# Performance work log

Measured on AMD Instinct MI355X. Metric: run time of the kernel, lower is better.

Reference implementation:

```python
import jax, jax.numpy as jnp
import numpy as np

HIDDEN = 2048
NUM_HEADS = 32
NUM_KV_HEADS = 8
HEAD_DIM = 64
HEADS_PER_KV = NUM_HEADS // NUM_KV_HEADS


def setup_inputs() -> dict:
    key = jax.random.key(0)
    ks = jax.random.split(key, 5)
    B, S = 2, 2048
    sd = 1.0 / np.sqrt(HIDDEN)
    x = jax.random.normal(ks[0], (B, S, HIDDEN), dtype=jnp.float32)
    wq = jax.random.normal(ks[1], (HIDDEN, NUM_HEADS * HEAD_DIM), dtype=jnp.float32) * sd
    wk = jax.random.normal(ks[2], (HIDDEN, NUM_KV_HEADS * HEAD_DIM), dtype=jnp.float32) * sd
    wv = jax.random.normal(ks[3], (HIDDEN, NUM_KV_HEADS * HEAD_DIM), dtype=jnp.float32) * sd
    wo = jax.random.normal(ks[4], (NUM_HEADS * HEAD_DIM, HIDDEN), dtype=jnp.float32) * sd
    return {"x": x, "wq": wq, "wk": wk, "wv": wv, "wo": wo}


def reference(x, wq, wk, wv, wo):
    B, S, _ = x.shape
    scale = 1.0 / np.sqrt(HEAD_DIM)
    # projections; self-attention (is_cross=False) so kv source = x
    q = (x @ wq).reshape(B, S, NUM_HEADS, HEAD_DIM)          # [B,S,H,D]
    k = (x @ wk).reshape(B, S, NUM_KV_HEADS, HEAD_DIM)        # [B,S,Hkv,D]
    v = (x @ wv).reshape(B, S, NUM_KV_HEADS, HEAD_DIM)
    # GQA: group query heads per kv head instead of repeating K/V
    q = q.reshape(B, S, NUM_KV_HEADS, HEADS_PER_KV, HEAD_DIM)
    # scores: [B, Hkv, G, Sq, Skv]
    scores = jnp.einsum('bqhgd,bkhd->bhgqk', q, k) * scale
    probs = jax.nn.softmax(scores, axis=-1)
    out = jnp.einsum('bhgqk,bkhd->bqhgd', probs, v)
    out = out.reshape(B, S, NUM_HEADS * HEAD_DIM)
    return out @ wo
```

## Files before the change

kernel.cpp:

```cpp
#include <hip/hip_runtime.h>
#include <hip/hip_bf16.h>


#define S_LEN 2048

typedef __hip_bfloat16 bf16;
using bf16x8 = __attribute__((ext_vector_type(8))) __bf16;
using f32x4  = __attribute__((ext_vector_type(4))) float;

__device__ inline unsigned short bf16_bits(float f) {
    union { __hip_bfloat16 h; unsigned short u; } cv;
    cv.h = __float2bfloat16(f);
    return cv.u;
}

__device__ inline float bits_to_f(unsigned short u) {
    union { __hip_bfloat16 h; unsigned short u; } cv;
    cv.u = u;
    return __bfloat162float(cv.h);
}

__device__ inline unsigned int cvt_pk_bf16(float lo, float hi) {
    unsigned int r;
    asm volatile("v_cvt_pk_bf16_f32 %0, %1, %2" : "=v"(r) : "v"(lo), "v"(hi));
    return r;
}

__device__ inline bf16x8 load_cvt8(const float* __restrict__ p) {
    f32x4 a = *(const f32x4*)p;
    f32x4 b = *(const f32x4*)(p + 4);
    union { bf16x8 v; unsigned short u[8]; } r;
    r.u[0] = bf16_bits(a[0]); r.u[1] = bf16_bits(a[1]);
    r.u[2] = bf16_bits(a[2]); r.u[3] = bf16_bits(a[3]);
    r.u[4] = bf16_bits(b[0]); r.u[5] = bf16_bits(b[1]);
    r.u[6] = bf16_bits(b[2]); r.u[7] = bf16_bits(b[3]);
    return r.v;
}

__device__ inline void gload_lds16(const bf16* g, bf16* l) {
    __builtin_amdgcn_global_load_lds((const __attribute__((address_space(1))) void*)g,
                                     (__attribute__((address_space(3))) void*)l,
                                     16, 0, 0);
}

__global__ __launch_bounds__(256) void prep_k(const float* __restrict__ x,
                                              const float* __restrict__ wq,
                                              const float* __restrict__ wk,
                                              const float* __restrict__ wv,
                                              bf16* __restrict__ xb,
                                              bf16* __restrict__ wqT,
                                              bf16* __restrict__ wkT,
                                              bf16* __restrict__ wvT) {
    __shared__ float tile[32][33];
    int bid = blockIdx.x;
    if (bid < 4096) {
        int i = bid * 256 + threadIdx.x;
        *(bf16x8*)(xb + (size_t)i * 8) = load_cvt8(x + (size_t)i * 8);
        return;
    }
    const float* in; bf16* out; int R, C, local;
    if (bid < 8192)      { local = bid - 4096; in = wq; out = wqT; R = 2048; C = 2048; }
    else if (bid < 9216) { local = bid - 8192; in = wk; out = wkT; R = 2048; C = 512;  }
    else                 { local = bid - 9216; in = wv; out = wvT; R = 2048; C = 512;  }
    int gx = C >> 5;
    int c0 = (local % gx) * 32, r0 = (local / gx) * 32;
    int tx = threadIdx.x & 31, ty = threadIdx.x >> 5;
#pragma unroll
    for (int p = 0; p < 4; ++p)
        tile[ty + p * 8][tx] = in[(size_t)(r0 + ty + p * 8) * C + c0 + tx];
    __syncthreads();
#pragma unroll
    for (int p = 0; p < 4; ++p)
        out[(size_t)(c0 + ty + p * 8) * R + r0 + tx] = __float2bfloat16(tile[tx][ty + p * 8]);
}

__global__ __launch_bounds__(256) void transpose_k(const float* __restrict__ in,
                                                   bf16* __restrict__ out,
                                                   int R, int C) {
    __shared__ float tile[32][33];
    int tx = threadIdx.x & 31, ty = threadIdx.x >> 5;
    int r0 = blockIdx.y * 32, c0 = blockIdx.x * 32;
#pragma unroll
    for (int p = 0; p < 4; ++p)
        tile[ty + p * 8][tx] = in[(size_t)(r0 + ty + p * 8) * C + c0 + tx];
    __syncthreads();
#pragma unroll
    for (int p = 0; p < 4; ++p)
        out[(size_t)(c0 + ty + p * 8) * R + r0 + tx] = __float2bfloat16(tile[tx][ty + p * 8]);
}

__global__ __launch_bounds__(256) void gemm_k(const bf16* __restrict__ A,
                                              const bf16* __restrict__ Bt,
                                              void* __restrict__ Cv,
                                              void* __restrict__ Cv2,
                                              void* __restrict__ Cv3,
                                              int M, int N, int K, int mode) {
    __shared__ bf16 As[128 * 32];
    __shared__ bf16 Bs[128 * 32];
    int tid  = threadIdx.x;
    int lane = tid & 63, wave = tid >> 6;
    int quad = lane >> 4, r = lane & 15;
    int wm = (wave >> 1) * 64, wn = (wave & 1) * 64;

    int nwg  = gridDim.x * gridDim.y;
    int flat = blockIdx.y * gridDim.x + blockIdx.x;
    int cpx  = nwg >> 3;
    int swz  = (flat & 7) * cpx + (flat >> 3);
    int m0 = (swz / gridDim.x) * 128, n0 = (swz % gridDim.x) * 128;

    f32x4 acc[4][4];
#pragma unroll
    for (int i = 0; i < 4; ++i)
#pragma unroll
        for (int j = 0; j < 4; ++j) acc[i][j] = (f32x4)0.0f;

    int rg = lane >> 2;
    int ck = (lane & 3) << 3;

    for (int k0 = 0; k0 < K; k0 += 32) {
#pragma unroll
        for (int g = 0; g < 2; ++g) {
            int grp = wave * 2 + g;
            int row = grp * 16 + rg;
            gload_lds16(A  + (size_t)(m0 + row) * K + k0 + ck, &As[grp * 512]);
            gload_lds16(Bt + (size_t)(n0 + row) * K + k0 + ck, &Bs[grp * 512]);
        }
        __syncthreads();
        bf16x8 af[4], bfr[4];
#pragma unroll
        for (int mt = 0; mt < 4; ++mt) af[mt]  = *(const bf16x8*)&As[(wm + mt * 16 + r) * 32 + quad * 8];
#pragma unroll
        for (int nt = 0; nt < 4; ++nt) bfr[nt] = *(const bf16x8*)&Bs[(wn + nt * 16 + r) * 32 + quad * 8];
#pragma unroll
        for (int mt = 0; mt < 4; ++mt)
#pragma unroll
            for (int nt = 0; nt < 4; ++nt)
                acc[mt][nt] = __builtin_amdgcn_mfma_f32_16x16x32_bf16(af[mt], bfr[nt], acc[mt][nt], 0, 0, 0);
        __syncthreads();
    }

    if (mode == 2) {
        float* C = (float*)Cv;
#pragma unroll
        for (int mt = 0; mt < 4; ++mt)
#pragma unroll
            for (int nt = 0; nt < 4; ++nt) {
                int row = m0 + wm + mt * 16 + quad * 4;
                int col = n0 + wn + nt * 16 + r;
#pragma unroll
                for (int i = 0; i < 4; ++i)
                    C[(size_t)(row + i) * N + col] = acc[mt][nt][i];
            }
    } else {
        if (n0 < 2048) {
            bf16* C = (bf16*)Cv;
#pragma unroll
            for (int mt = 0; mt < 4; ++mt)
#pragma unroll
                for (int nt = 0; nt < 4; ++nt) {
                    int row = m0 + wm + mt * 16 + quad * 4;
                    int col = n0 + wn + nt * 16 + r;
#pragma unroll
                    for (int i = 0; i < 4; ++i)
                        C[(size_t)(row + i) * 2048 + col] = __float2bfloat16(acc[mt][nt][i]);
                }
        } else if (n0 < 2560) {
            bf16* C = (bf16*)Cv2;
#pragma unroll
            for (int mt = 0; mt < 4; ++mt)
#pragma unroll
                for (int nt = 0; nt < 4; ++nt) {
                    int row = m0 + wm + mt * 16 + quad * 4;
                    int col = n0 - 2048 + wn + nt * 16 + r;
#pragma unroll
                    for (int i = 0; i < 4; ++i)
                        C[(size_t)(row + i) * 512 + col] = __float2bfloat16(acc[mt][nt][i]);
                }
        } else {
            unsigned short* C = (unsigned short*)Cv3;
#pragma unroll
            for (int mt = 0; mt < 4; ++mt)
#pragma unroll
                for (int nt = 0; nt < 4; ++nt) {
                    int rowb = m0 + wm + mt * 16 + quad * 4;
                    int col  = n0 - 2560 + wn + nt * 16 + r;
                    int b = rowb >> 11, s = rowb & 2047;
                    ushort4 pk;
                    pk.x = bf16_bits(acc[mt][nt][0]);
                    pk.y = bf16_bits(acc[mt][nt][1]);
                    pk.z = bf16_bits(acc[mt][nt][2]);
                    pk.w = bf16_bits(acc[mt][nt][3]);
                    *(ushort4*)(C + (size_t)(b * 512 + col) * 2048 + s) = pk;
                }
        }
    }
}

__global__ __launch_bounds__(256) void attn_k(const bf16* __restrict__ Qin,
                                              const bf16* __restrict__ Kb,
                                              const bf16* __restrict__ Vt,
                                              bf16* __restrict__ Aout) {
    __shared__ bf16 Ks[2][64 * 64];
    __shared__ bf16 Vs[2][64 * 64];
    __shared__ bf16 Pl[4][16 * 64];

    int tid = threadIdx.x, lane = tid & 63, w = tid >> 6;
    int quad = lane >> 4, r = lane & 15;
    int qt = blockIdx.x, h = blockIdx.y, b = blockIdx.z;
    int hk = h >> 2;
    int q0 = qt * 64 + w * 16;

    bf16x8 qf[2];
#pragma unroll
    for (int f = 0; f < 2; ++f) {
        bf16x8 v = *(const bf16x8*)(Qin + (size_t)(b * S_LEN + q0 + r) * 2048 + h * 64 + f * 32 + quad * 8);
        union { bf16x8 v; unsigned short u[8]; } in_, out_;
        in_.v = v;
#pragma unroll
        for (int j = 0; j < 8; ++j) out_.u[j] = bf16_bits(bits_to_f(in_.u[j]) * 0.125f);
        qf[f] = out_.v;
    }

    bf16x8 onesf;
    {
        union { bf16x8 v; unsigned short u[8]; } o_;
#pragma unroll
        for (int j = 0; j < 8; ++j) o_.u[j] = 0x3F80;
        onesf = o_.v;
    }

    const bf16* Kbase = Kb + (size_t)b * S_LEN * 512 + hk * 64;
    const bf16* Vbase = Vt + (size_t)(b * 512 + hk * 64) * 2048;
    char* myP = (char*)&Pl[w][0];

    int srow   = lane >> 3;
    int schunk = (lane & 7) ^ srow;
    int wrow0 = w * 16, wrow1 = w * 16 + 8;

    f32x4 oacc[4];
#pragma unroll
    for (int dt = 0; dt < 4; ++dt) oacc[dt] = (f32x4)0.0f;
    f32x4 lacc = (f32x4)0.0f;

    gload_lds16(Kbase + (size_t)(wrow0 + srow) * 512 + schunk * 8, &Ks[0][wrow0 * 64]);
    gload_lds16(Kbase + (size_t)(wrow1 + srow) * 512 + schunk * 8, &Ks[0][wrow1 * 64]);
    gload_lds16(Vbase + (size_t)(wrow0 + srow) * 2048 + 0 + schunk * 8, &Vs[0][wrow0 * 64]);
    gload_lds16(Vbase + (size_t)(wrow1 + srow) * 2048 + 0 + schunk * 8, &Vs[0][wrow1 * 64]);
    __syncthreads();

#define ATTN_STEP(BUF, K0)                                                               \
    do {                                                                                 \
        int k0n_ = (K0) + 64;                                                            \
        if (k0n_ < S_LEN) {                                                              \
            gload_lds16(Kbase + (size_t)(k0n_ + wrow0 + srow) * 512 + schunk * 8,        \
                        &Ks[(BUF) ^ 1][wrow0 * 64]);                                     \
            gload_lds16(Kbase + (size_t)(k0n_ + wrow1 + srow) * 512 + schunk * 8,        \
                        &Ks[(BUF) ^ 1][wrow1 * 64]);                                     \
            gload_lds16(Vbase + (size_t)(wrow0 + srow) * 2048 + k0n_ + schunk * 8,       \
                        &Vs[(BUF) ^ 1][wrow0 * 64]);                                     \
            gload_lds16(Vbase + (size_t)(wrow1 + srow) * 2048 + k0n_ + schunk * 8,       \
                        &Vs[(BUF) ^ 1][wrow1 * 64]);                                     \
        }                                                                                \
        bf16x8 kf[4][2];                                                                 \
        for (int t = 0; t < 4; ++t)                                                      \
            for (int half = 0; half < 2; ++half)                                         \
                kf[t][half] = *(const bf16x8*)&Ks[BUF][(t * 16 + r) * 64 +               \
                                                ((half * 4 + quad) ^ (r & 7)) * 8];      \
        f32x4 St[4];                                                                     \
        __builtin_amdgcn_s_setprio(1);                                                   \
        for (int t = 0; t < 4; ++t) {                                                    \
            St[t] = (f32x4)0.0f;                                                         \
            St[t] = __builtin_amdgcn_mfma_f32_16x16x32_bf16(kf[t][0], qf[0], St[t], 0, 0, 0); \
            St[t] = __builtin_amdgcn_mfma_f32_16x16x32_bf16(kf[t][1], qf[1], St[t], 0, 0, 0); \
        }                                                                                \
        __builtin_amdgcn_s_setprio(0);                                                   \
             \
        float p[16];                                                                     \
        for (int t = 0; t < 4; ++t)                                                      \
            for (int i = 0; i < 4; ++i) p[t * 4 + i] = __expf(St[t][i]);                 \
        for (int t = 0; t < 4; ++t) {                                                    \
            uint2 pk;                                                                    \
            pk.x = cvt_pk_bf16(p[t * 4 + 0], p[t * 4 + 1]);                              \
            pk.y = cvt_pk_bf16(p[t * 4 + 2], p[t * 4 + 3]);                              \
            *(uint2*)(myP + r * 128 + (((t * 2 + (quad >> 1)) ^ (r & 7)) * 16) +         \
                      (quad & 1) * 8) = pk;                                              \
        }                                                                                \
        bf16x8 pf0 = *(const bf16x8*)(myP + r * 128 + ((quad ^ (r & 7)) * 16));          \
        bf16x8 pf1 = *(const bf16x8*)(myP + r * 128 + (((4 + quad) ^ (r & 7)) * 16));    \
        bf16x8 vf[4][2];                                                                 \
        for (int dt = 0; dt < 4; ++dt)                                                   \
            for (int half = 0; half < 2; ++half)                                         \
                vf[dt][half] = *(const bf16x8*)&Vs[BUF][(dt * 16 + r) * 64 +             \
                                                ((half * 4 + quad) ^ (r & 7)) * 8];      \
        __builtin_amdgcn_s_setprio(1);                                                   \
        lacc = __builtin_amdgcn_mfma_f32_16x16x32_bf16(pf0, onesf, lacc, 0, 0, 0);       \
        lacc = __builtin_amdgcn_mfma_f32_16x16x32_bf16(pf1, onesf, lacc, 0, 0, 0);       \
        for (int dt = 0; dt < 4; ++dt) {                                                 \
            f32x4 o = oacc[dt];                                                          \
            o = __builtin_amdgcn_mfma_f32_16x16x32_bf16(pf0, vf[dt][0], o, 0, 0, 0);     \
            o = __builtin_amdgcn_mfma_f32_16x16x32_bf16(pf1, vf[dt][1], o, 0, 0, 0);     \
            oacc[dt] = o;                                                                \
        }                                                                                \
        __builtin_amdgcn_s_setprio(0);                                                   \
        __syncthreads();                                                                 \
    } while (0)

    for (int itp = 0; itp < S_LEN / 128; ++itp) {
        int base = itp * 128;
        ATTN_STEP(0, base);
        ATTN_STEP(1, base + 64);
    }
#undef ATTN_STEP

    float linv[4];
#pragma unroll
    for (int i = 0; i < 4; ++i) linv[i] = 1.0f / lacc[i];
#pragma unroll
    for (int dt = 0; dt < 4; ++dt)
#pragma unroll
        for (int i = 0; i < 4; ++i)
            Aout[(size_t)(b * S_LEN + q0 + quad * 4 + i) * 2048 + h * 64 + dt * 16 + r] =
                __float2bfloat16(oacc[dt][i] * linv[i]);
}

extern "C" void kernel_launch(void* const* d_in, const int* in_sizes, int n_in,
                              void* d_out, int out_size, void* d_ws, size_t ws_size,
                              hipStream_t stream) {
    const float* x  = (const float*)d_in[0];
    const float* wq = (const float*)d_in[1];
    const float* wk = (const float*)d_in[2];
    const float* wv = (const float*)d_in[3];
    const float* wo = (const float*)d_in[4];
    char* ws = (char*)d_ws;

    bf16* wqT  = (bf16*)(ws + 0);
    bf16* wkT  = (bf16*)(ws + 8388608);
    bf16* wvT  = (bf16*)(ws + 10485760);
    bf16* attn = (bf16*)(ws + 0);
    bf16* Kb   = (bf16*)(ws + 16777216);
    bf16* Vtb  = (bf16*)(ws + 20971520);
    bf16* woT  = (bf16*)(ws + 16777216);
    bf16* Qb   = (bf16*)d_out;
    bf16* xb   = (bf16*)((char*)d_out + 16777216);

    prep_k<<<dim3(10240), 256, 0, stream>>>(x, wq, wk, wv, xb, wqT, wkT, wvT);

    gemm_k<<<dim3(24, 32), 256, 0, stream>>>(xb, wqT, Qb, Kb, Vtb, 4096, 3072, 2048, 3);

    attn_k<<<dim3(32, 32, 2), 256, 0, stream>>>(Qb, Kb, Vtb, attn);

    transpose_k<<<dim3(64, 64), 256, 0, stream>>>(wo, woT, 2048, 2048);

    gemm_k<<<dim3(16, 32), 256, 0, stream>>>(attn, woT, d_out, nullptr, nullptr, 4096, 2048, 2048, 2);
}
```

Measured before the change: 347.9 us.

## Process two query tiles per attention block to reuse K/V tiles

Each attention workgroup now handles 128 query rows instead of 64: every wave keeps two sets of Q fragments, accumulators and row sums. Each K/V tile staged in LDS and each K fragment read from LDS is reused for both query tiles, which halves global K/V traffic and LDS K reads per query. The grid is halved to 16x32x2 blocks. The cost is higher register pressure, lower occupancy and fewer blocks to spread across CUs.

```diff
diff --git a/kernel.cpp b/kernel.cpp
--- a/kernel.cpp
+++ b/kernel.cpp
@@ -208,17 +208,22 @@
     int quad = lane >> 4, r = lane & 15;
     int qt = blockIdx.x, h = blockIdx.y, b = blockIdx.z;
     int hk = h >> 2;
-    int q0 = qt * 64 + w * 16;
-
-    bf16x8 qf[2];
+    int qA = qt * 128 + w * 16;
+    int qB = qA + 64;
+
+    bf16x8 qfA[2], qfB[2];
 #pragma unroll
     for (int f = 0; f < 2; ++f) {
-        bf16x8 v = *(const bf16x8*)(Qin + (size_t)(b * S_LEN + q0 + r) * 2048 + h * 64 + f * 32 + quad * 8);
-        union { bf16x8 v; unsigned short u[8]; } in_, out_;
-        in_.v = v;
-#pragma unroll
-        for (int j = 0; j < 8; ++j) out_.u[j] = bf16_bits(bits_to_f(in_.u[j]) * 0.125f);
-        qf[f] = out_.v;
+        bf16x8 vA = *(const bf16x8*)(Qin + (size_t)(b * S_LEN + qA + r) * 2048 + h * 64 + f * 32 + quad * 8);
+        bf16x8 vB = *(const bf16x8*)(Qin + (size_t)(b * S_LEN + qB + r) * 2048 + h * 64 + f * 32 + quad * 8);
+        union { bf16x8 v; unsigned short u[8]; } ia, oa, ib, ob;
+        ia.v = vA; ib.v = vB;
+#pragma unroll
+        for (int j = 0; j < 8; ++j) {
+            oa.u[j] = bf16_bits(bits_to_f(ia.u[j]) * 0.125f);
+            ob.u[j] = bf16_bits(bits_to_f(ib.u[j]) * 0.125f);
+        }
+        qfA[f] = oa.v; qfB[f] = ob.v;
     }
 
     bf16x8 onesf;
@@ -237,16 +242,42 @@
     int schunk = (lane & 7) ^ srow;
     int wrow0 = w * 16, wrow1 = w * 16 + 8;
 
-    f32x4 oacc[4];
-#pragma unroll
-    for (int dt = 0; dt < 4; ++dt) oacc[dt] = (f32x4)0.0f;
-    f32x4 lacc = (f32x4)0.0f;
+    f32x4 oA[4], oB[4];
+#pragma unroll
+    for (int dt = 0; dt < 4; ++dt) { oA[dt] = (f32x4)0.0f; oB[dt] = (f32x4)0.0f; }
+    f32x4 laccA = (f32x4)0.0f, laccB = (f32x4)0.0f;
 
     gload_lds16(Kbase + (size_t)(wrow0 + srow) * 512 + schunk * 8, &Ks[0][wrow0 * 64]);
     gload_lds16(Kbase + (size_t)(wrow1 + srow) * 512 + schunk * 8, &Ks[0][wrow1 * 64]);
     gload_lds16(Vbase + (size_t)(wrow0 + srow) * 2048 + 0 + schunk * 8, &Vs[0][wrow0 * 64]);
     gload_lds16(Vbase + (size_t)(wrow1 + srow) * 2048 + 0 + schunk * 8, &Vs[0][wrow1 * 64]);
     __syncthreads();
+
+#define SM_PV(Sv, LACC, OACC)                                                            \
+    do {                                                                                 \
+        float p[16];                                                                     \
+        for (int t = 0; t < 4; ++t)                                                      \
+            for (int i = 0; i < 4; ++i) p[t * 4 + i] = __expf(Sv[t][i]);                 \
+        for (int t = 0; t < 4; ++t) {                                                    \
+            uint2 pk;                                                                    \
+            pk.x = cvt_pk_bf16(p[t * 4 + 0], p[t * 4 + 1]);                              \
+            pk.y = cvt_pk_bf16(p[t * 4 + 2], p[t * 4 + 3]);                              \
+            *(uint2*)(myP + r * 128 + (((t * 2 + (quad >> 1)) ^ (r & 7)) * 16) +         \
+                      (quad & 1) * 8) = pk;                                              \
+        }                                                                                \
+        bf16x8 pf0 = *(const bf16x8*)(myP + r * 128 + ((quad ^ (r & 7)) * 16));          \
+        bf16x8 pf1 = *(const bf16x8*)(myP + r * 128 + (((4 + quad) ^ (r & 7)) * 16));    \
+        __builtin_amdgcn_s_setprio(1);                                                   \
+        LACC = __builtin_amdgcn_mfma_f32_16x16x32_bf16(pf0, onesf, LACC, 0, 0, 0);       \
+        LACC = __builtin_amdgcn_mfma_f32_16x16x32_bf16(pf1, onesf, LACC, 0, 0, 0);       \
+        for (int dt = 0; dt < 4; ++dt) {                                                 \
+            f32x4 o = OACC[dt];                                                          \
+            o = __builtin_amdgcn_mfma_f32_16x16x32_bf16(pf0, vf[dt][0], o, 0, 0, 0);     \
+            o = __builtin_amdgcn_mfma_f32_16x16x32_bf16(pf1, vf[dt][1], o, 0, 0, 0);     \
+            OACC[dt] = o;                                                                \
+        }                                                                                \
+        __builtin_amdgcn_s_setprio(0);                                                   \
+    } while (0)
 
 #define ATTN_STEP(BUF, K0)                                                               \
     do {                                                                                 \
@@ -261,47 +292,33 @@
             gload_lds16(Vbase + (size_t)(wrow1 + srow) * 2048 + k0n_ + schunk * 8,       \
                         &Vs[(BUF) ^ 1][wrow1 * 64]);                                     \
         }                                                                                \
-        bf16x8 kf[4][2];                                                                 \
-        for (int t = 0; t < 4; ++t)                                                      \
-            for (int half = 0; half < 2; ++half)                                         \
-                kf[t][half] = *(const bf16x8*)&Ks[BUF][(t * 16 + r) * 64 +               \
-                                                ((half * 4 + quad) ^ (r & 7)) * 8];      \
-        f32x4 St[4];                                                                     \
-        __builtin_amdgcn_s_setprio(1);                                                   \
-        for (int t = 0; t < 4; ++t) {                                                    \
-            St[t] = (f32x4)0.0f;                                                         \
-            St[t] = __builtin_amdgcn_mfma_f32_16x16x32_bf16(kf[t][0], qf[0], St[t], 0, 0, 0); \
-            St[t] = __builtin_amdgcn_mfma_f32_16x16x32_bf16(kf[t][1], qf[1], St[t], 0, 0, 0); \
+        f32x4 SA[4], SB[4];                                                              \
+        {                                                                                \
+            bf16x8 kf[4][2];                                                             \
+            for (int t = 0; t < 4; ++t)                                                  \
+                for (int half = 0; half < 2; ++half)                                     \
+                    kf[t][half] = *(const bf16x8*)&Ks[BUF][(t * 16 + r) * 64 +           \
+                                                    ((half * 4 + quad) ^ (r & 7)) * 8];  \
+            __builtin_amdgcn_s_setprio(1);                                               \
+            for (int t = 0; t < 4; ++t) {                                                \
+                SA[t] = (f32x4)0.0f;                                                     \
+                SA[t] = __builtin_amdgcn_mfma_f32_16x16x32_bf16(kf[t][0], qfA[0], SA[t], 0, 0, 0); \
+                SA[t] = __builtin_amdgcn_mfma_f32_16x16x32_bf16(kf[t][1], qfA[1], SA[t], 0, 0, 0); \
+            }                                                                            \
+            for (int t = 0; t < 4; ++t) {                                                \
+                SB[t] = (f32x4)0.0f;                                                     \
+                SB[t] = __builtin_amdgcn_mfma_f32_16x16x32_bf16(kf[t][0], qfB[0], SB[t], 0, 0, 0); \
+                SB[t] = __builtin_amdgcn_mfma_f32_16x16x32_bf16(kf[t][1], qfB[1], SB[t], 0, 0, 0); \
+            }                                                                            \
+            __builtin_amdgcn_s_setprio(0);                                               \
         }                                                                                \
-        __builtin_amdgcn_s_setprio(0);                                                   \
-             \
-        float p[16];                                                                     \
-        for (int t = 0; t < 4; ++t)                                                      \
-            for (int i = 0; i < 4; ++i) p[t * 4 + i] = __expf(St[t][i]);                 \
-        for (int t = 0; t < 4; ++t) {                                                    \
-            uint2 pk;                                                                    \
-            pk.x = cvt_pk_bf16(p[t * 4 + 0], p[t * 4 + 1]);                              \
-            pk.y = cvt_pk_bf16(p[t * 4 + 2], p[t * 4 + 3]);                              \
-            *(uint2*)(myP + r * 128 + (((t * 2 + (quad >> 1)) ^ (r & 7)) * 16) +         \
-                      (quad & 1) * 8) = pk;                                              \
-        }                                                                                \
-        bf16x8 pf0 = *(const bf16x8*)(myP + r * 128 + ((quad ^ (r & 7)) * 16));          \
-        bf16x8 pf1 = *(const bf16x8*)(myP + r * 128 + (((4 + quad) ^ (r & 7)) * 16));    \
         bf16x8 vf[4][2];                                                                 \
         for (int dt = 0; dt < 4; ++dt)                                                   \
             for (int half = 0; half < 2; ++half)                                         \
                 vf[dt][half] = *(const bf16x8*)&Vs[BUF][(dt * 16 + r) * 64 +             \
                                                 ((half * 4 + quad) ^ (r & 7)) * 8];      \
-        __builtin_amdgcn_s_setprio(1);                                                   \
-        lacc = __builtin_amdgcn_mfma_f32_16x16x32_bf16(pf0, onesf, lacc, 0, 0, 0);       \
-        lacc = __builtin_amdgcn_mfma_f32_16x16x32_bf16(pf1, onesf, lacc, 0, 0, 0);       \
-        for (int dt = 0; dt < 4; ++dt) {                                                 \
-            f32x4 o = oacc[dt];                                                          \
-            o = __builtin_amdgcn_mfma_f32_16x16x32_bf16(pf0, vf[dt][0], o, 0, 0, 0);     \
-            o = __builtin_amdgcn_mfma_f32_16x16x32_bf16(pf1, vf[dt][1], o, 0, 0, 0);     \
-            oacc[dt] = o;                                                                \
-        }                                                                                \
-        __builtin_amdgcn_s_setprio(0);                                                   \
+        SM_PV(SA, laccA, oA);                                                            \
+        SM_PV(SB, laccB, oB);                                                            \
         __syncthreads();                                                                 \
     } while (0)
 
@@ -311,16 +328,23 @@
         ATTN_STEP(1, base + 64);
     }
 #undef ATTN_STEP
-
-    float linv[4];
-#pragma unroll
-    for (int i = 0; i < 4; ++i) linv[i] = 1.0f / lacc[i];
+#undef SM_PV
+
+    float linvA[4], linvB[4];
+#pragma unroll
+    for (int i = 0; i < 4; ++i) {
+        linvA[i] = 1.0f / laccA[i];
+        linvB[i] = 1.0f / laccB[i];
+    }
 #pragma unroll
     for (int dt = 0; dt < 4; ++dt)
 #pragma unroll
-        for (int i = 0; i < 4; ++i)
-            Aout[(size_t)(b * S_LEN + q0 + quad * 4 + i) * 2048 + h * 64 + dt * 16 + r] =
-                __float2bfloat16(oacc[dt][i] * linv[i]);
+        for (int i = 0; i < 4; ++i) {
+            Aout[(size_t)(b * S_LEN + qA + quad * 4 + i) * 2048 + h * 64 + dt * 16 + r] =
+                __float2bfloat16(oA[dt][i] * linvA[i]);
+            Aout[(size_t)(b * S_LEN + qB + quad * 4 + i) * 2048 + h * 64 + dt * 16 + r] =
+                __float2bfloat16(oB[dt][i] * linvB[i]);
+        }
 }
 
 extern "C" void kernel_launch(void* const* d_in, const int* in_sizes, int n_in,
@@ -347,7 +371,7 @@
 
     gemm_k<<<dim3(24, 32), 256, 0, stream>>>(xb, wqT, Qb, Kb, Vtb, 4096, 3072, 2048, 3);
 
-    attn_k<<<dim3(32, 32, 2), 256, 0, stream>>>(Qb, Kb, Vtb, attn);
+    attn_k<<<dim3(16, 32, 2), 256, 0, stream>>>(Qb, Kb, Vtb, attn);
 
     transpose_k<<<dim3(64, 64), 256, 0, stream>>>(wo, woT, 2048, 2048);
 
```

New measurement: 337.7 us. 2.9% less time.

## Process four query sub-tiles per attention block to reuse K/V tiles

Applied to the files above, without the earlier changes.

Each attention block now handles 256 query rows, four 64-row sub-tiles, instead of 64, so every K/V tile loaded into LDS feeds four times as many MFMAs. The grid shrinks from 32 to 8 query tiles per head and batch. This cuts global K/V traffic and per-tile load and sync overhead. In exchange it raises register pressure with four sets of accumulators and query fragments, adds a launch-bounds occupancy hint, and leaves fewer blocks in the grid.

```diff
diff --git a/kernel.cpp b/kernel.cpp
--- a/kernel.cpp
+++ b/kernel.cpp
@@ -196,10 +196,10 @@
     }
 }
 
-__global__ __launch_bounds__(256) void attn_k(const bf16* __restrict__ Qin,
-                                              const bf16* __restrict__ Kb,
-                                              const bf16* __restrict__ Vt,
-                                              bf16* __restrict__ Aout) {
+__global__ __launch_bounds__(256, 2) void attn_k(const bf16* __restrict__ Qin,
+                                                 const bf16* __restrict__ Kb,
+                                                 const bf16* __restrict__ Vt,
+                                                 bf16* __restrict__ Aout) {
     __shared__ bf16 Ks[2][64 * 64];
     __shared__ bf16 Vs[2][64 * 64];
     __shared__ bf16 Pl[4][16 * 64];
@@ -208,17 +208,20 @@
     int quad = lane >> 4, r = lane & 15;
     int qt = blockIdx.x, h = blockIdx.y, b = blockIdx.z;
     int hk = h >> 2;
-    int q0 = qt * 64 + w * 16;
-
-    bf16x8 qf[2];
-#pragma unroll
-    for (int f = 0; f < 2; ++f) {
-        bf16x8 v = *(const bf16x8*)(Qin + (size_t)(b * S_LEN + q0 + r) * 2048 + h * 64 + f * 32 + quad * 8);
-        union { bf16x8 v; unsigned short u[8]; } in_, out_;
-        in_.v = v;
-#pragma unroll
-        for (int j = 0; j < 8; ++j) out_.u[j] = bf16_bits(bits_to_f(in_.u[j]) * 0.125f);
-        qf[f] = out_.v;
+
+    bf16x8 qf[4][2];
+#pragma unroll
+    for (int s = 0; s < 4; ++s) {
+        int q0 = qt * 256 + s * 64 + w * 16;
+#pragma unroll
+        for (int f = 0; f < 2; ++f) {
+            bf16x8 v = *(const bf16x8*)(Qin + (size_t)(b * S_LEN + q0 + r) * 2048 + h * 64 + f * 32 + quad * 8);
+            union { bf16x8 v; unsigned short u[8]; } i_, o_;
+            i_.v = v;
+#pragma unroll
+            for (int j = 0; j < 8; ++j) o_.u[j] = bf16_bits(bits_to_f(i_.u[j]) * 0.125f);
+            qf[s][f] = o_.v;
+        }
     }
 
     bf16x8 onesf;
@@ -237,10 +240,14 @@
     int schunk = (lane & 7) ^ srow;
     int wrow0 = w * 16, wrow1 = w * 16 + 8;
 
-    f32x4 oacc[4];
-#pragma unroll
-    for (int dt = 0; dt < 4; ++dt) oacc[dt] = (f32x4)0.0f;
-    f32x4 lacc = (f32x4)0.0f;
+    f32x4 oacc[4][4];
+#pragma unroll
+    for (int s = 0; s < 4; ++s)
+#pragma unroll
+        for (int dt = 0; dt < 4; ++dt) oacc[s][dt] = (f32x4)0.0f;
+    f32x4 lacc[4];
+#pragma unroll
+    for (int s = 0; s < 4; ++s) lacc[s] = (f32x4)0.0f;
 
     gload_lds16(Kbase + (size_t)(wrow0 + srow) * 512 + schunk * 8, &Ks[0][wrow0 * 64]);
     gload_lds16(Kbase + (size_t)(wrow1 + srow) * 512 + schunk * 8, &Ks[0][wrow1 * 64]);
@@ -261,47 +268,63 @@
             gload_lds16(Vbase + (size_t)(wrow1 + srow) * 2048 + k0n_ + schunk * 8,       \
                         &Vs[(BUF) ^ 1][wrow1 * 64]);                                     \
         }                                                                                \
-        bf16x8 kf[4][2];                                                                 \
-        for (int t = 0; t < 4; ++t)                                                      \
-            for (int half = 0; half < 2; ++half)                                         \
-                kf[t][half] = *(const bf16x8*)&Ks[BUF][(t * 16 + r) * 64 +               \
-                                                ((half * 4 + quad) ^ (r & 7)) * 8];      \
-        f32x4 St[4];                                                                     \
-        __builtin_amdgcn_s_setprio(1);                                                   \
-        for (int t = 0; t < 4; ++t) {                                                    \
-            St[t] = (f32x4)0.0f;                                                         \
-            St[t] = __builtin_amdgcn_mfma_f32_16x16x32_bf16(kf[t][0], qf[0], St[t], 0, 0, 0); \
-            St[t] = __builtin_amdgcn_mfma_f32_16x16x32_bf16(kf[t][1], qf[1], St[t], 0, 0, 0); \
+        f32x4 S[4][4];                                                                   \
+        {                                                                                \
+            bf16x8 kf[4][2];                                                             \
+            _Pragma("unroll")                                                            \
+            for (int t = 0; t < 4; ++t)                                                  \
+                _Pragma("unroll")                                                        \
+                for (int half = 0; half < 2; ++half)                                     \
+                    kf[t][half] = *(const bf16x8*)&Ks[BUF][(t * 16 + r) * 64 +           \
+                                                    ((half * 4 + quad) ^ (r & 7)) * 8];  \
+            __builtin_amdgcn_s_setprio(1);                                               \
+            _Pragma("unroll")                                                            \
+            for (int s = 0; s < 4; ++s)                                                  \
+                _Pragma("unroll")                                                        \
+                for (int t = 0; t < 4; ++t) {                                            \
+                    f32x4 z = (f32x4)0.0f;                                               \
+                    z = __builtin_amdgcn_mfma_f32_16x16x32_bf16(kf[t][0], qf[s][0], z, 0, 0, 0); \
+                    z = __builtin_amdgcn_mfma_f32_16x16x32_bf16(kf[t][1], qf[s][1], z, 0, 0, 0); \
+                    S[s][t] = z;                                                         \
+                }                                                                        \
+            __builtin_amdgcn_s_setprio(0);                                               \
         }                                                                                \
-        __builtin_amdgcn_s_setprio(0);                                                   \
-             \
-        float p[16];                                                                     \
-        for (int t = 0; t < 4; ++t)                                                      \
-            for (int i = 0; i < 4; ++i) p[t * 4 + i] = __expf(St[t][i]);                 \
-        for (int t = 0; t < 4; ++t) {                                                    \
-            uint2 pk;                                                                    \
-            pk.x = cvt_pk_bf16(p[t * 4 + 0], p[t * 4 + 1]);                              \
-            pk.y = cvt_pk_bf16(p[t * 4 + 2], p[t * 4 + 3]);                              \
-            *(uint2*)(myP + r * 128 + (((t * 2 + (quad >> 1)) ^ (r & 7)) * 16) +         \
-                      (quad & 1) * 8) = pk;                                              \
-        }                                                                                \
-        bf16x8 pf0 = *(const bf16x8*)(myP + r * 128 + ((quad ^ (r & 7)) * 16));          \
-        bf16x8 pf1 = *(const bf16x8*)(myP + r * 128 + (((4 + quad) ^ (r & 7)) * 16));    \
         bf16x8 vf[4][2];                                                                 \
+        _Pragma("unroll")                                                                \
         for (int dt = 0; dt < 4; ++dt)                                                   \
+            _Pragma("unroll")                                                            \
             for (int half = 0; half < 2; ++half)                                         \
                 vf[dt][half] = *(const bf16x8*)&Vs[BUF][(dt * 16 + r) * 64 +             \
                                                 ((half * 4 + quad) ^ (r & 7)) * 8];      \
-        __builtin_amdgcn_s_setprio(1);                                                   \
-        lacc = __builtin_amdgcn_mfma_f32_16x16x32_bf16(pf0, onesf, lacc, 0, 0, 0);       \
-        lacc = __builtin_amdgcn_mfma_f32_16x16x32_bf16(pf1, onesf, lacc, 0, 0, 0);       \
-        for (int dt = 0; dt < 4; ++dt) {                                                 \
-            f32x4 o = oacc[dt];                                                          \
-            o = __builtin_amdgcn_mfma_f32_16x16x32_bf16(pf0, vf[dt][0], o, 0, 0, 0);     \
-            o = __builtin_amdgcn_mfma_f32_16x16x32_bf16(pf1, vf[dt][1], o, 0, 0, 0);     \
-            oacc[dt] = o;                                                                \
+        _Pragma("unroll")                                                                \
+        for (int s = 0; s < 4; ++s) {                                                    \
+            float p[16];                                                                 \
+            _Pragma("unroll")                                                            \
+            for (int t = 0; t < 4; ++t)                                                  \
+                _Pragma("unroll")                                                        \
+                for (int i = 0; i < 4; ++i) p[t * 4 + i] = __expf(S[s][t][i]);           \
+            _Pragma("unroll")                                                            \
+            for (int t = 0; t < 4; ++t) {                                                \
+                uint2 pk;                                                                \
+                pk.x = cvt_pk_bf16(p[t * 4 + 0], p[t * 4 + 1]);                          \
+                pk.y = cvt_pk_bf16(p[t * 4 + 2], p[t * 4 + 3]);                          \
+                *(uint2*)(myP + r * 128 + (((t * 2 + (quad >> 1)) ^ (r & 7)) * 16) +     \
+                          (quad & 1) * 8) = pk;                                          \
+            }                                                                            \
+            bf16x8 pf0 = *(const bf16x8*)(myP + r * 128 + ((quad ^ (r & 7)) * 16));      \
+            bf16x8 pf1 = *(const bf16x8*)(myP + r * 128 + (((4 + quad) ^ (r & 7)) * 16));\
+            __builtin_amdgcn_s_setprio(1);                                               \
+            lacc[s] = __builtin_amdgcn_mfma_f32_16x16x32_bf16(pf0, onesf, lacc[s], 0, 0, 0); \
+            lacc[s] = __builtin_amdgcn_mfma_f32_16x16x32_bf16(pf1, onesf, lacc[s], 0, 0, 0); \
+            _Pragma("unroll")                                                            \
+            for (int dt = 0; dt < 4; ++dt) {                                             \
+                f32x4 o = oacc[s][dt];                                                   \
+                o = __builtin_amdgcn_mfma_f32_16x16x32_bf16(pf0, vf[dt][0], o, 0, 0, 0); \
+                o = __builtin_amdgcn_mfma_f32_16x16x32_bf16(pf1, vf[dt][1], o, 0, 0, 0); \
+                oacc[s][dt] = o;                                                         \
+            }                                                                            \
+            __builtin_amdgcn_s_setprio(0);                                               \
         }                                                                                \
-        __builtin_amdgcn_s_setprio(0);                                                   \
         __syncthreads();                                                                 \
     } while (0)
 
@@ -312,15 +335,19 @@
     }
 #undef ATTN_STEP
 
-    float linv[4];
-#pragma unroll
-    for (int i = 0; i < 4; ++i) linv[i] = 1.0f / lacc[i];
-#pragma unroll
-    for (int dt = 0; dt < 4; ++dt)
-#pragma unroll
-        for (int i = 0; i < 4; ++i)
-            Aout[(size_t)(b * S_LEN + q0 + quad * 4 + i) * 2048 + h * 64 + dt * 16 + r] =
-                __float2bfloat16(oacc[dt][i] * linv[i]);
+#pragma unroll
+    for (int s = 0; s < 4; ++s) {
+        int q0 = qt * 256 + s * 64 + w * 16;
+        float linv[4];
+#pragma unroll
+        for (int i = 0; i < 4; ++i) linv[i] = 1.0f / lacc[s][i];
+#pragma unroll
+        for (int dt = 0; dt < 4; ++dt)
+#pragma unroll
+            for (int i = 0; i < 4; ++i)
+                Aout[(size_t)(b * S_LEN + q0 + quad * 4 + i) * 2048 + h * 64 + dt * 16 + r] =
+                    __float2bfloat16(oacc[s][dt][i] * linv[i]);
+    }
 }
 
 extern "C" void kernel_launch(void* const* d_in, const int* in_sizes, int n_in,
@@ -347,7 +374,7 @@
 
     gemm_k<<<dim3(24, 32), 256, 0, stream>>>(xb, wqT, Qb, Kb, Vtb, 4096, 3072, 2048, 3);
 
-    attn_k<<<dim3(32, 32, 2), 256, 0, stream>>>(Qb, Kb, Vtb, attn);
+    attn_k<<<dim3(8, 32, 2), 256, 0, stream>>>(Qb, Kb, Vtb, attn);
 
     transpose_k<<<dim3(64, 64), 256, 0, stream>>>(wo, woT, 2048, 2048);
 
```

New measurement: 320.4 us (median of 2 runs). -7.9%, faster.
